# Optimization experiments

Hardware: AMD Instinct MI355X
Metric: run time of the kernel (lower is better)

Reference implementation:

```python
import jax, jax.numpy as jnp
from jax import lax
import numpy as np

B, C, H, W = 32, 256, 56, 56
G1, G2 = 64, 4          # groups for 3x3 convs, number of parallel convs / 1x1 groups
EPS = 1e-5
DN = ('NCHW', 'OIHW', 'NCHW')


def setup_inputs() -> dict:
    key = jax.random.key(0)
    it = iter(jax.random.split(key, 32))
    nk = lambda: next(it)
    n = lambda shape, s=0.05: jax.random.normal(nk(), shape, jnp.float32) * s
    u = lambda shape: jax.random.uniform(nk(), shape, jnp.float32, minval=0.5, maxval=1.5)
    inp = {'x': jax.random.normal(nk(), (B, C, H, W), jnp.float32)}
    inp.update(
        w1=n((G2, G1, C // G1, 3, 3), 0.1), b1=n((G2, G1)),
        bn1a_g=1.0 + n((C,)), bn1a_b=n((C,)), bn1a_m=n((C,)), bn1a_v=u((C,)),
        pw1=n((C, C // G2, 1, 1), 0.1), pb1=n((C,)),
        bn1b_g=1.0 + n((C,)), bn1b_b=n((C,)), bn1b_m=n((C,)), bn1b_v=u((C,)),
        w2=n((G2, G1, C // G1, 3, 3), 0.1), b2=n((G2, G1)),
        bn2a_g=1.0 + n((C,)), bn2a_b=n((C,)), bn2a_m=n((C,)), bn2a_v=u((C,)),
        pw2=n((C, C // G2, 1, 1), 0.1), pb2=n((C,)),
        bn2b_g=1.0 + n((C,)), bn2b_b=n((C,)), bn2b_m=n((C,)), bn2b_v=u((C,)),
    )
    return inp


def _bn_relu(x, g, b, m, v):
    # inference-mode BatchNorm2d + ReLU, fused into one affine + relu
    inv = g / jnp.sqrt(v + EPS)
    return jax.nn.relu(x * inv[None, :, None, None] + (b - m * inv)[None, :, None, None])


def _gconv3x3(x, w, b):
    # Faithful to: [Conv2d(Cin, g1, k=3, p=1, groups=g1) for _ in range(g2)] then concat(dim=1).
    # Implemented as ONE grouped conv (feature_group_count=g1) followed by a cheap channel permute
    # to recover torch's concat ordering (conv-index major, group minor).
    g2, g1, cpg = w.shape[0], w.shape[1], w.shape[2]
    # combined weight: out channel k*g2 + i (group-major) uses conv i, group k
    Wc = jnp.transpose(w, (1, 0, 2, 3, 4)).reshape(g1 * g2, cpg, 3, 3)
    y = lax.conv_general_dilated(x, Wc, (1, 1), ((1, 1), (1, 1)),
                                 feature_group_count=g1, dimension_numbers=DN)
    Bx, _, Hy, Wy = y.shape
    # (g, i) ordering -> torch concat (i, g) ordering
    y = y.reshape(Bx, g1, g2, Hy, Wy).transpose(0, 2, 1, 3, 4).reshape(Bx, g1 * g2, Hy, Wy)
    return y + b.reshape(g1 * g2)[None, :, None, None]


def _pwconv(x, w, b):
    # Conv2d(C, C, k=1, groups=G2)
    y = lax.conv_general_dilated(x, w, (1, 1), 'VALID',
                                 feature_group_count=G2, dimension_numbers=DN)
    return y + b[None, :, None, None]


def reference(x, w1, b1, bn1a_g, bn1a_b, bn1a_m, bn1a_v, pw1, pb1,
              bn1b_g, bn1b_b, bn1b_m, bn1b_v,
              w2, b2, bn2a_g, bn2a_b, bn2a_m, bn2a_v, pw2, pb2,
              bn2b_g, bn2b_b, bn2b_m, bn2b_v):
    h = _gconv3x3(x, w1, b1)
    h = _bn_relu(h, bn1a_g, bn1a_b, bn1a_m, bn1a_v)
    h = _pwconv(h, pw1, pb1)
    h = _bn_relu(h, bn1b_g, bn1b_b, bn1b_m, bn1b_v)
    h = _gconv3x3(h, w2, b2)
    h = _bn_relu(h, bn2a_g, bn2a_b, bn2a_m, bn2a_v)
    h = _pwconv(h, pw2, pb2)
    h = _bn_relu(h, bn2b_g, bn2b_b, bn2b_m, bn2b_v)
    return h
```

## Files before the change

kernel.cpp:

```cpp
#include <hip/hip_runtime.h>

#define HW 3136
#define SHS 120

__global__ __launch_bounds__(256, 5) void fused_stage(
    const float* __restrict__ in,
    const float* __restrict__ gw,
    const float* __restrict__ gb,
    const float* __restrict__ bnag, const float* __restrict__ bnab,
    const float* __restrict__ bnam, const float* __restrict__ bnav,
    const float* __restrict__ pw,
    const float* __restrict__ pb,
    const float* __restrict__ bnbg, const float* __restrict__ bnbb,
    const float* __restrict__ bnbm, const float* __restrict__ bnbv,
    float* __restrict__ out)
{
    __shared__ float sH[64 * SHS];

    const int tid = threadIdx.x;

    const int idx  = blockIdx.x;
    const int xcd  = idx & 7;
    const int qq   = idx >> 3;
    const int g    = qq & 3;
    const int slot = qq >> 2;
    const int u    = slot * 8 + xcd;
    const int b    = u / 28;
    const int t    = u - b * 28;
    const int y0   = t * 2;

    const int k  = tid >> 2;
    const int xs = tid & 3;
    const int x0 = xs * 14;

    float acc[2][14];
#pragma unroll
    for (int r = 0; r < 2; ++r)
#pragma unroll
        for (int xx = 0; xx < 14; ++xx) acc[r][xx] = 0.f;

    const float* wkp = gw + (size_t)(g * 64 + k) * 36;

#pragma unroll
    for (int cc = 0; cc < 4; ++cc) {
        float wr9[9];
#pragma unroll
        for (int j = 0; j < 9; ++j) wr9[j] = wkp[cc * 9 + j];
        const float* chp = in + ((size_t)(b * 256 + k * 4 + cc)) * HW;
#pragma unroll
        for (int ry = 0; ry < 4; ++ry) {
            const int gy = y0 - 1 + ry;
            if ((unsigned)gy >= 56u) continue;
            const float* rp = chp + gy * 56;
            float rr[16];
            rr[0]  = (x0 > 0)       ? rp[x0 - 1]  : 0.f;
            rr[15] = (x0 + 14 < 56) ? rp[x0 + 14] : 0.f;
#pragma unroll
            for (int j = 0; j < 7; ++j) {
                float2 v = *(const float2*)(rp + x0 + 2 * j);
                rr[1 + 2*j] = v.x; rr[2 + 2*j] = v.y;
            }
#pragma unroll
            for (int r = 0; r < 2; ++r) {
                const int wi = ry - r;
                if (wi < 0 || wi > 2) continue;
                const float w0 = wr9[wi*3 + 0];
                const float w1 = wr9[wi*3 + 1];
                const float w2 = wr9[wi*3 + 2];
#pragma unroll
                for (int xx = 0; xx < 14; ++xx)
                    acc[r][xx] = fmaf(w2, rr[xx+2],
                                 fmaf(w1, rr[xx+1],
                                 fmaf(w0, rr[xx], acc[r][xx])));
            }
        }
    }

    {
        const int c = g * 64 + k;
        const float sc = bnag[c] * rsqrtf(bnav[c] + 1e-5f);
        const float sh = fmaf(gb[c], sc, bnab[c] - bnam[c] * sc);
#pragma unroll
        for (int r = 0; r < 2; ++r)
#pragma unroll
            for (int j = 0; j < 7; ++j) {
                float v0 = fmaxf(fmaf(acc[r][2*j],   sc, sh), 0.f);
                float v1 = fmaxf(fmaf(acc[r][2*j+1], sc, sh), 0.f);
                *(float2*)&sH[k * SHS + r * 56 + x0 + 2*j] = make_float2(v0, v1);
            }
    }
    __syncthreads();

    const int og = tid >> 3;
    const int pg = tid & 7;
    const int p0 = pg * 14;

    float a2[2][14];
#pragma unroll
    for (int i = 0; i < 2; ++i)
#pragma unroll
        for (int xx = 0; xx < 14; ++xx) a2[i][xx] = 0.f;

    const float* wp0 = pw + (size_t)(g * 64 + og * 2) * 64;

#pragma unroll 2
    for (int c = 0; c < 64; c += 4) {
        const float4 w0 = *(const float4*)(wp0 + c);
        const float4 w1 = *(const float4*)(wp0 + 64 + c);
        const float w0a[4] = {w0.x, w0.y, w0.z, w0.w};
        const float w1a[4] = {w1.x, w1.y, w1.z, w1.w};
#pragma unroll
        for (int q2 = 0; q2 < 4; ++q2) {
            float hr[14];
#pragma unroll
            for (int j = 0; j < 7; ++j) {
                float2 v = *(const float2*)&sH[(c + q2) * SHS + p0 + 2*j];
                hr[2*j] = v.x; hr[2*j+1] = v.y;
            }
            const float wa = w0a[q2];
            const float wb = w1a[q2];
#pragma unroll
            for (int xx = 0; xx < 14; ++xx) {
                a2[0][xx] = fmaf(wa, hr[xx], a2[0][xx]);
                a2[1][xx] = fmaf(wb, hr[xx], a2[1][xx]);
            }
        }
    }

    const int orow = y0 + ((p0 >= 56) ? 1 : 0);
    const int ox   = (p0 >= 56) ? p0 - 56 : p0;
#pragma unroll
    for (int i = 0; i < 2; ++i) {
        const int o = g * 64 + og * 2 + i;
        const float sc = bnbg[o] * rsqrtf(bnbv[o] + 1e-5f);
        const float sh = fmaf(pb[o], sc, bnbb[o] - bnbm[o] * sc);
        float* op = out + ((size_t)(b * 256 + o)) * HW + orow * 56 + ox;
#pragma unroll
        for (int j = 0; j < 7; ++j) {
            float v0 = fmaxf(fmaf(a2[i][2*j],   sc, sh), 0.f);
            float v1 = fmaxf(fmaf(a2[i][2*j+1], sc, sh), 0.f);
            *(float2*)(op + 2*j) = make_float2(v0, v1);
        }
    }
}

extern "C" void kernel_launch(void* const* d_in, const int* in_sizes, int n_in,
                              void* d_out, int out_size, void* d_ws, size_t ws_size,
                              hipStream_t stream) {
    const float* x     = (const float*)d_in[0];
    const float* w1    = (const float*)d_in[1];
    const float* b1    = (const float*)d_in[2];
    const float* bn1ag = (const float*)d_in[3];
    const float* bn1ab = (const float*)d_in[4];
    const float* bn1am = (const float*)d_in[5];
    const float* bn1av = (const float*)d_in[6];
    const float* pw1   = (const float*)d_in[7];
    const float* pb1   = (const float*)d_in[8];
    const float* bn1bg = (const float*)d_in[9];
    const float* bn1bb = (const float*)d_in[10];
    const float* bn1bm = (const float*)d_in[11];
    const float* bn1bv = (const float*)d_in[12];
    const float* w2    = (const float*)d_in[13];
    const float* b2    = (const float*)d_in[14];
    const float* bn2ag = (const float*)d_in[15];
    const float* bn2ab = (const float*)d_in[16];
    const float* bn2am = (const float*)d_in[17];
    const float* bn2av = (const float*)d_in[18];
    const float* pw2   = (const float*)d_in[19];
    const float* pb2   = (const float*)d_in[20];
    const float* bn2bg = (const float*)d_in[21];
    const float* bn2bb = (const float*)d_in[22];
    const float* bn2bm = (const float*)d_in[23];
    const float* bn2bv = (const float*)d_in[24];

    float* mid  = (float*)d_ws;
    float* outp = (float*)d_out;

    const int grid = 32 * 4 * 28;

    fused_stage<<<grid, 256, 0, stream>>>(x,   w1, b1, bn1ag, bn1ab, bn1am, bn1av,
                                          pw1, pb1, bn1bg, bn1bb, bn1bm, bn1bv, mid);
    fused_stage<<<grid, 256, 0, stream>>>(mid, w2, b2, bn2ag, bn2ab, bn2am, bn2av,
                                          pw2, pb2, bn2bg, bn2bb, bn2bm, bn2bv, outp);
}
```

Before: 496.6 us.

## Map 3x3 grouped conv to lane-per-column with shuffles and interleave pointwise pixel mapping

The grouped 3x3 conv stage is restructured so that each wavefront loops over 16 output channels, with each lane owning one image column and pulling horizontal neighbours via cross-lane shuffles instead of per-thread register row strips. The pointwise stage switches from contiguous 14-pixel chunks per thread to a strided interleaved pixel mapping, which improves LDS and global store coalescing. Launch bounds occupancy drops from 5 to 4, and one unroll pragma is removed. The change lowers register pressure and makes global loads coalesced per lane, but it adds shuffle overhead and a serial channel loop, and 8 of the 64 lanes sit idle in the conv stage.

Measured after the change: 517.1 us. +4.1%, slower.

```diff
diff --git a/kernel.cpp b/kernel.cpp
--- a/kernel.cpp
+++ b/kernel.cpp
@@ -3,7 +3,7 @@
 #define HW 3136
 #define SHS 120
 
-__global__ __launch_bounds__(256, 5) void fused_stage(
+__global__ __launch_bounds__(256, 4) void fused_stage(
     const float* __restrict__ in,
     const float* __restrict__ gw,
     const float* __restrict__ gb,
@@ -29,71 +29,68 @@
     const int t    = u - b * 28;
     const int y0   = t * 2;
 
-    const int k  = tid >> 2;
-    const int xs = tid & 3;
-    const int x0 = xs * 14;
+    const int l  = tid & 63;
+    const int wv = __builtin_amdgcn_readfirstlane(tid >> 6);
+    const int p  = l - 1;
+    const bool pok = (unsigned)p < 56u;
 
-    float acc[2][14];
+    for (int kk = 0; kk < 16; ++kk) {
+        const int k = wv * 16 + kk;
+
+        float wr[36];
+        {
+            const float4* w4 = (const float4*)(gw + (size_t)(g * 64 + k) * 36);
 #pragma unroll
-    for (int r = 0; r < 2; ++r)
-#pragma unroll
-        for (int xx = 0; xx < 14; ++xx) acc[r][xx] = 0.f;
+            for (int j = 0; j < 9; ++j) {
+                float4 v = w4[j];
+                wr[4*j+0] = v.x; wr[4*j+1] = v.y; wr[4*j+2] = v.z; wr[4*j+3] = v.w;
+            }
+        }
 
-    const float* wkp = gw + (size_t)(g * 64 + k) * 36;
+        float acc0 = 0.f, acc1 = 0.f;
+        const float* chp0 = in + ((size_t)(b * 256 + k * 4)) * HW;
 
 #pragma unroll
-    for (int cc = 0; cc < 4; ++cc) {
-        float wr9[9];
+        for (int cc = 0; cc < 4; ++cc) {
+            const float* chp = chp0 + cc * HW;
+            float vrow[4];
 #pragma unroll
-        for (int j = 0; j < 9; ++j) wr9[j] = wkp[cc * 9 + j];
-        const float* chp = in + ((size_t)(b * 256 + k * 4 + cc)) * HW;
-#pragma unroll
-        for (int ry = 0; ry < 4; ++ry) {
-            const int gy = y0 - 1 + ry;
-            if ((unsigned)gy >= 56u) continue;
-            const float* rp = chp + gy * 56;
-            float rr[16];
-            rr[0]  = (x0 > 0)       ? rp[x0 - 1]  : 0.f;
-            rr[15] = (x0 + 14 < 56) ? rp[x0 + 14] : 0.f;
-#pragma unroll
-            for (int j = 0; j < 7; ++j) {
-                float2 v = *(const float2*)(rp + x0 + 2 * j);
-                rr[1 + 2*j] = v.x; rr[2 + 2*j] = v.y;
+            for (int ry = 0; ry < 4; ++ry) {
+                const int gy = y0 - 1 + ry;
+                float v = 0.f;
+                if ((unsigned)gy < 56u && pok) v = chp[gy * 56 + p];
+                vrow[ry] = v;
             }
 #pragma unroll
-            for (int r = 0; r < 2; ++r) {
-                const int wi = ry - r;
-                if (wi < 0 || wi > 2) continue;
-                const float w0 = wr9[wi*3 + 0];
-                const float w1 = wr9[wi*3 + 1];
-                const float w2 = wr9[wi*3 + 2];
+            for (int ry = 0; ry < 4; ++ry) {
+                const float a  = vrow[ry];
+                const float b1 = __shfl_down(a, 1);
+                const float b2 = __shfl_down(a, 2);
 #pragma unroll
-                for (int xx = 0; xx < 14; ++xx)
-                    acc[r][xx] = fmaf(w2, rr[xx+2],
-                                 fmaf(w1, rr[xx+1],
-                                 fmaf(w0, rr[xx], acc[r][xx])));
+                for (int r = 0; r < 2; ++r) {
+                    const int wi = ry - r;
+                    if (wi < 0 || wi > 2) continue;
+                    const float w0 = wr[cc*9 + wi*3 + 0];
+                    const float w1 = wr[cc*9 + wi*3 + 1];
+                    const float w2 = wr[cc*9 + wi*3 + 2];
+                    const float s  = fmaf(w2, b2, fmaf(w1, b1, w0 * a));
+                    if (r == 0) acc0 += s; else acc1 += s;
+                }
             }
         }
-    }
 
-    {
         const int c = g * 64 + k;
         const float sc = bnag[c] * rsqrtf(bnav[c] + 1e-5f);
         const float sh = fmaf(gb[c], sc, bnab[c] - bnam[c] * sc);
-#pragma unroll
-        for (int r = 0; r < 2; ++r)
-#pragma unroll
-            for (int j = 0; j < 7; ++j) {
-                float v0 = fmaxf(fmaf(acc[r][2*j],   sc, sh), 0.f);
-                float v1 = fmaxf(fmaf(acc[r][2*j+1], sc, sh), 0.f);
-                *(float2*)&sH[k * SHS + r * 56 + x0 + 2*j] = make_float2(v0, v1);
-            }
+        if (l < 56) {
+            sH[k * SHS + l]      = fmaxf(fmaf(acc0, sc, sh), 0.f);
+            sH[k * SHS + 56 + l] = fmaxf(fmaf(acc1, sc, sh), 0.f);
+        }
     }
     __syncthreads();
 
     const int og = tid >> 3;
     const int pg = tid & 7;
-    const int p0 = pg * 14;
 
     float a2[2][14];
 #pragma unroll
@@ -103,7 +100,6 @@
 
     const float* wp0 = pw + (size_t)(g * 64 + og * 2) * 64;
 
-#pragma unroll 2
     for (int c = 0; c < 64; c += 4) {
         const float4 w0 = *(const float4*)(wp0 + c);
         const float4 w1 = *(const float4*)(wp0 + 64 + c);
@@ -114,7 +110,7 @@
             float hr[14];
 #pragma unroll
             for (int j = 0; j < 7; ++j) {
-                float2 v = *(const float2*)&sH[(c + q2) * SHS + p0 + 2*j];
+                float2 v = *(const float2*)&sH[(c + q2) * SHS + 16*j + 2*pg];
                 hr[2*j] = v.x; hr[2*j+1] = v.y;
             }
             const float wa = w0a[q2];
@@ -127,19 +123,17 @@
         }
     }
 
-    const int orow = y0 + ((p0 >= 56) ? 1 : 0);
-    const int ox   = (p0 >= 56) ? p0 - 56 : p0;
 #pragma unroll
     for (int i = 0; i < 2; ++i) {
         const int o = g * 64 + og * 2 + i;
         const float sc = bnbg[o] * rsqrtf(bnbv[o] + 1e-5f);
         const float sh = fmaf(pb[o], sc, bnbb[o] - bnbm[o] * sc);
-        float* op = out + ((size_t)(b * 256 + o)) * HW + orow * 56 + ox;
+        float* op = out + ((size_t)(b * 256 + o)) * HW + y0 * 56;
 #pragma unroll
         for (int j = 0; j < 7; ++j) {
             float v0 = fmaxf(fmaf(a2[i][2*j],   sc, sh), 0.f);
             float v1 = fmaxf(fmaf(a2[i][2*j+1], sc, sh), 0.f);
-            *(float2*)(op + 2*j) = make_float2(v0, v1);
+            *(float2*)(op + 16*j + 2*pg) = make_float2(v0, v1);
         }
     }
 }
```
